# Optimization experiments

Measured on AMD Instinct MI355X. Metric: run time of the kernel, lower is better.

The kernel has to match this reference:

```python
import jax, jax.numpy as jnp
import numpy as np

RADIUS = 1.0
NSAMPLE = 1024  # num_votes
EPS = 1e-5     # BatchNorm eps


def _bn2(x, gamma, beta):
    # BatchNorm over [B, C, NS]: stats per channel across (batch, sample)
    m = jnp.mean(x, axis=(0, 2), keepdims=True)
    v = jnp.var(x, axis=(0, 2), keepdims=True)
    return gamma[None, :, None] * (x - m) * jax.lax.rsqrt(v + EPS) + beta[None, :, None]


def _bn1(x, gamma, beta):
    # BatchNorm over [B, C] (conv1d head with length 1): stats across batch
    m = jnp.mean(x, axis=0, keepdims=True)
    v = jnp.var(x, axis=0, keepdims=True)
    return gamma[None, :] * (x - m) * jax.lax.rsqrt(v + EPS) + beta[None, :]


def setup_inputs() -> dict:
    key = jax.random.key(0)
    ks = jax.random.split(key, 16)
    B, N, C = 8, 65536, 256
    def w(k, o, i):
        return jax.random.normal(k, (o, i), jnp.float32) * (1.0 / np.sqrt(i))
    inp = {
        'xyz': jax.random.normal(ks[0], (B, N, 3), jnp.float32),
        'features': jax.random.normal(ks[1], (B, C, N), jnp.float32),
        # shared MLP (conv2d 1x1 + BN + ReLU) x3, input channels = C+3 (use_xyz)
        'w1': w(ks[2], 128, C + 3), 'b1': jnp.zeros(128), 'g1': jnp.ones(128), 'be1': jnp.zeros(128),
        'w2': w(ks[3], 128, 128),   'b2': jnp.zeros(128), 'g2': jnp.ones(128), 'be2': jnp.zeros(128),
        'w3': w(ks[4], 128, 128),   'b3': jnp.zeros(128), 'g3': jnp.ones(128), 'be3': jnp.zeros(128),
        # conv1d head
        'hw1': w(ks[5], 128, 128), 'hb1': jnp.zeros(128), 'hg1': jnp.ones(128), 'hbe1': jnp.zeros(128),
        'hw2': w(ks[6], 128, 128), 'hb2': jnp.zeros(128), 'hg2': jnp.ones(128), 'hbe2': jnp.zeros(128),
        'hw3': w(ks[7], 12, 128),  'hb3': jnp.zeros(12),
    }
    return inp


def reference(xyz, features, w1, b1, g1, be1, w2, b2, g2, be2, w3, b3, g3, be3,
              hw1, hb1, hg1, hbe1, hw2, hb2, hg2, hbe2, hw3, hb3):
    B, N, _ = xyz.shape
    # FPS with npoint=1 deterministically selects point 0
    center = xyz[:, 0, :]                                   # [B,3]
    d2 = jnp.sum((xyz - center[:, None, :]) ** 2, axis=-1)   # [B,N]
    mask = d2 < RADIUS * RADIUS
    ar = jnp.arange(N)
    # ball query: first NSAMPLE in-radius indices (index order), pad with first hit
    order = jnp.argsort(jnp.where(mask, ar, N + ar), axis=1)[:, :NSAMPLE]  # [B,NS]
    valid = jnp.take_along_axis(mask, order, axis=1)
    inds = jnp.where(valid, order, order[:, :1])              # [B,NS]
    g_xyz = (jnp.take_along_axis(xyz, inds[:, :, None], axis=1) - center[:, None, :]) / RADIUS  # [B,NS,3]
    g_feat = jax.vmap(lambda f, i: f[:, i])(features, inds)    # [B,C,NS]
    g = jnp.concatenate([jnp.swapaxes(g_xyz, 1, 2), g_feat], axis=1)  # [B,C+3,NS]

    def mlp(x, w, b, gm, bt):
        y = jnp.einsum('oc,bcn->bon', w, x) + b[None, :, None]
        return jax.nn.relu(_bn2(y, gm, bt))

    h = mlp(g, w1, b1, g1, be1)
    h = mlp(h, w2, b2, g2, be2)
    h = mlp(h, w3, b3, g3, be3)
    f = jnp.max(h, axis=2)                                    # [B,128] maxpool over nsample

    net = jax.nn.relu(_bn1(f @ hw1.T + hb1, hg1, hbe1))
    net = jax.nn.relu(_bn1(net @ hw2.T + hb2, hg2, hbe2))
    net = net @ hw3.T + hb3                                   # [B,12]

    center_out = center + net[:, 0:3]
    size = net[:, 3:6]
    rot_6d = net[:, 6:12]
    return (center_out, size, rot_6d)
```

## Files before the change

### kernel.cpp

```cpp
#include <hip/hip_runtime.h>
#include <hip/hip_bf16.h>
#include <stdint.h>

#define BATCH 8
#define NPTS  65536
#define CFEAT 256
#define K1    259
#define CH    128
#define NS    1024
#define EPSF  1e-5f

__global__ __launch_bounds__(1024) void k_select(const float* __restrict__ xyz,
                                                 int* __restrict__ inds,
                                                 float* __restrict__ center) {
  int b = blockIdx.x;
  int tid = threadIdx.x;
  int lane = tid & 63, wid = tid >> 6;
  const float* xb = xyz + (size_t)b * NPTS * 3;
  float cx = xb[0], cy = xb[1], cz = xb[2];
  if (tid < 3) center[b * 3 + tid] = xb[tid];

  __shared__ int wcnt[16];
  int total = 0;
  int* ib = inds + b * NS;

  for (int base = 0; base < NPTS; base += 1024) {
    int i = base + tid;
    float dx = xb[(size_t)i * 3 + 0] - cx;
    float dy = xb[(size_t)i * 3 + 1] - cy;
    float dz = xb[(size_t)i * 3 + 2] - cz;
    float d2 = dx * dx + dy * dy + dz * dz;
    bool pred = d2 < 1.0f;
    unsigned long long bal = __ballot(pred);
    if (lane == 0) wcnt[wid] = (int)__popcll(bal);
    __syncthreads();
    int woff = 0, itot = 0;
#pragma unroll
    for (int w = 0; w < 16; ++w) {
      int c = wcnt[w];
      if (w < wid) woff += c;
      itot += c;
    }
    int pos = total + woff + (int)__popcll(bal & ((1ull << lane) - 1ull));
    if (pred && pos < NS) ib[pos] = i;
    total += itot;
    __syncthreads();
    if (total >= NS) break;
  }
  for (int j = total + tid; j < NS; j += 1024) ib[j] = 0;
}

__global__ __launch_bounds__(256) void k_gather(const float* __restrict__ xyz,
                                                const float* __restrict__ feat,
                                                const int* __restrict__ inds,
                                                const float* __restrict__ center,
                                                float* __restrict__ g) {
  int bc = blockIdx.x;
  int b = bc / K1, c = bc % K1;
  const int* ib = inds + b * NS;
  float* gout = g + ((size_t)b * K1 + c) * NS;
  if (c < 3) {
    float cen = center[b * 3 + c];
    for (int n = threadIdx.x; n < NS; n += 256) {
      int id = ib[n];
      gout[n] = xyz[((size_t)b * NPTS + id) * 3 + c] - cen;
    }
  } else {
    const float* fr = feat + ((size_t)b * CFEAT + (c - 3)) * NPTS;
    for (int n = threadIdx.x; n < NS; n += 256) {
      gout[n] = fr[ib[n]];
    }
  }
}

__global__ __launch_bounds__(256) void k_gemm1(const float* __restrict__ g,
                                               const float* __restrict__ W,
                                               const float* __restrict__ bias,
                                               float* __restrict__ y) {
  __shared__ float Ws[128 * 32];
  __shared__ float Xs[32 * 64];
  int b = blockIdx.y;
  int n0 = blockIdx.x * 64;
  int tid = threadIdx.x;
  int tx = tid & 15, ty = tid >> 4;
  float acc[8][4];
#pragma unroll
  for (int r = 0; r < 8; ++r)
#pragma unroll
    for (int j = 0; j < 4; ++j) acc[r][j] = 0.f;

  const float* xb = g + (size_t)b * K1 * NS;
  for (int k0 = 0; k0 < K1; k0 += 32) {
    for (int e = tid; e < 128 * 32; e += 256) {
      int o = e >> 5, kk = e & 31;
      int k = k0 + kk;
      Ws[e] = (k < K1) ? W[o * K1 + k] : 0.f;
    }
    for (int e = tid; e < 32 * 64; e += 256) {
      int kk = e >> 6, j = e & 63;
      int k = k0 + kk;
      Xs[e] = (k < K1) ? xb[(size_t)k * NS + n0 + j] : 0.f;
    }
    __syncthreads();
#pragma unroll
    for (int kk = 0; kk < 32; ++kk) {
      float4 xv = *(const float4*)&Xs[kk * 64 + tx * 4];
#pragma unroll
      for (int r = 0; r < 8; ++r) {
        float a = Ws[(ty * 8 + r) * 32 + kk];
        acc[r][0] += a * xv.x;
        acc[r][1] += a * xv.y;
        acc[r][2] += a * xv.z;
        acc[r][3] += a * xv.w;
      }
    }
    __syncthreads();
  }
#pragma unroll
  for (int r = 0; r < 8; ++r) {
    int o = ty * 8 + r;
    float bs = bias[o];
    float4 v = make_float4(acc[r][0] + bs, acc[r][1] + bs, acc[r][2] + bs, acc[r][3] + bs);
    *(float4*)&y[((size_t)b * CH + o) * NS + n0 + tx * 4] = v;
  }
}

__global__ __launch_bounds__(256) void k_gemm23(const float* __restrict__ x,
                                                const float* __restrict__ scale,
                                                const float* __restrict__ shift,
                                                const float* __restrict__ W,
                                                const float* __restrict__ bias,
                                                float* __restrict__ y) {
  __shared__ float Ws[128 * 32];
  __shared__ float Xs[32 * 64];
  int b = blockIdx.y;
  int n0 = blockIdx.x * 64;
  int tid = threadIdx.x;
  int tx = tid & 15, ty = tid >> 4;
  float acc[8][4];
#pragma unroll
  for (int r = 0; r < 8; ++r)
#pragma unroll
    for (int j = 0; j < 4; ++j) acc[r][j] = 0.f;

  for (int k0 = 0; k0 < 128; k0 += 32) {
    for (int e = tid; e < 128 * 32; e += 256) {
      int o = e >> 5, kk = e & 31;
      Ws[e] = W[o * 128 + k0 + kk];
    }
    for (int e = tid; e < 32 * 64; e += 256) {
      int kk = e >> 6, j = e & 63;
      int k = k0 + kk;
      float v = x[((size_t)b * CH + k) * NS + n0 + j];
      Xs[e] = fmaxf(scale[k] * v + shift[k], 0.f);
    }
    __syncthreads();
#pragma unroll
    for (int kk = 0; kk < 32; ++kk) {
      float4 xv = *(const float4*)&Xs[kk * 64 + tx * 4];
#pragma unroll
      for (int r = 0; r < 8; ++r) {
        float a = Ws[(ty * 8 + r) * 32 + kk];
        acc[r][0] += a * xv.x;
        acc[r][1] += a * xv.y;
        acc[r][2] += a * xv.z;
        acc[r][3] += a * xv.w;
      }
    }
    __syncthreads();
  }
#pragma unroll
  for (int r = 0; r < 8; ++r) {
    int o = ty * 8 + r;
    float bs = bias[o];
    float4 v = make_float4(acc[r][0] + bs, acc[r][1] + bs, acc[r][2] + bs, acc[r][3] + bs);
    *(float4*)&y[((size_t)b * CH + o) * NS + n0 + tx * 4] = v;
  }
}

__global__ __launch_bounds__(256) void k_stats(const float* __restrict__ y,
                                               const float* __restrict__ gamma,
                                               const float* __restrict__ beta,
                                               float* __restrict__ scale,
                                               float* __restrict__ shift) {
  int c = blockIdx.x;
  int tid = threadIdx.x;
  float s = 0.f, sq = 0.f;
  for (int b = 0; b < BATCH; ++b) {
    const float* yr = y + ((size_t)b * CH + c) * NS;
    for (int n = tid; n < NS; n += 256) {
      float v = yr[n];
      s += v;
      sq += v * v;
    }
  }
  __shared__ float rs[256];
  __shared__ float rq[256];
  rs[tid] = s;
  rq[tid] = sq;
  __syncthreads();
  for (int st = 128; st > 0; st >>= 1) {
    if (tid < st) {
      rs[tid] += rs[tid + st];
      rq[tid] += rq[tid + st];
    }
    __syncthreads();
  }
  if (tid == 0) {
    const float inv = 1.f / (BATCH * NS);
    float mean = rs[0] * inv;
    float var = rq[0] * inv - mean * mean;
    if (var < 0.f) var = 0.f;
    float r = rsqrtf(var + EPSF);
    float sc = gamma[c] * r;
    scale[c] = sc;
    shift[c] = beta[c] - mean * sc;
  }
}

__global__ __launch_bounds__(256) void k_max(const float* __restrict__ y,
                                             const float* __restrict__ scale,
                                             const float* __restrict__ shift,
                                             float* __restrict__ f) {
  int idx = blockIdx.x;
  int c = idx & (CH - 1);
  const float* yr = y + (size_t)idx * NS;
  float sc = scale[c], sh = shift[c];
  float m = -1e30f;
  for (int n = threadIdx.x; n < NS; n += 256) m = fmaxf(m, sc * yr[n] + sh);
#pragma unroll
  for (int o = 32; o > 0; o >>= 1) m = fmaxf(m, __shfl_down(m, o, 64));
  __shared__ float wm[4];
  if ((threadIdx.x & 63) == 0) wm[threadIdx.x >> 6] = m;
  __syncthreads();
  if (threadIdx.x == 0) {
    m = fmaxf(fmaxf(wm[0], wm[1]), fmaxf(wm[2], wm[3]));
    f[idx] = fmaxf(m, 0.f);
  }
}

__global__ __launch_bounds__(128) void k_head(const float* __restrict__ f,
                                              const float* __restrict__ hw1, const float* __restrict__ hb1,
                                              const float* __restrict__ hg1, const float* __restrict__ hbe1,
                                              const float* __restrict__ hw2, const float* __restrict__ hb2,
                                              const float* __restrict__ hg2, const float* __restrict__ hbe2,
                                              const float* __restrict__ hw3, const float* __restrict__ hb3,
                                              const float* __restrict__ center,
                                              float* __restrict__ out) {
  __shared__ float A[BATCH * 128];
  __shared__ float Bm[BATCH * 128];
  int c = threadIdx.x;
  for (int b = 0; b < BATCH; ++b) A[b * 128 + c] = f[b * 128 + c];
  __syncthreads();

  {
    float v[BATCH];
    float bs = hb1[c];
#pragma unroll
    for (int b = 0; b < BATCH; ++b) v[b] = bs;
    for (int k = 0; k < 128; ++k) {
      float w = hw1[c * 128 + k];
#pragma unroll
      for (int b = 0; b < BATCH; ++b) v[b] += A[b * 128 + k] * w;
    }
    float m = 0.f;
#pragma unroll
    for (int b = 0; b < BATCH; ++b) m += v[b];
    m *= (1.f / BATCH);
    float var = 0.f;
#pragma unroll
    for (int b = 0; b < BATCH; ++b) { float d = v[b] - m; var += d * d; }
    var *= (1.f / BATCH);
    float r = rsqrtf(var + EPSF);
    float ga = hg1[c], be = hbe1[c];
#pragma unroll
    for (int b = 0; b < BATCH; ++b)
      Bm[b * 128 + c] = fmaxf(ga * (v[b] - m) * r + be, 0.f);
  }
  __syncthreads();

  {
    float v[BATCH];
    float bs = hb2[c];
#pragma unroll
    for (int b = 0; b < BATCH; ++b) v[b] = bs;
    for (int k = 0; k < 128; ++k) {
      float w = hw2[c * 128 + k];
#pragma unroll
      for (int b = 0; b < BATCH; ++b) v[b] += Bm[b * 128 + k] * w;
    }
    float m = 0.f;
#pragma unroll
    for (int b = 0; b < BATCH; ++b) m += v[b];
    m *= (1.f / BATCH);
    float var = 0.f;
#pragma unroll
    for (int b = 0; b < BATCH; ++b) { float d = v[b] - m; var += d * d; }
    var *= (1.f / BATCH);
    float r = rsqrtf(var + EPSF);
    float ga = hg2[c], be = hbe2[c];
#pragma unroll
    for (int b = 0; b < BATCH; ++b)
      A[b * 128 + c] = fmaxf(ga * (v[b] - m) * r + be, 0.f);
  }
  __syncthreads();

  if (c < 96) {
    int b = c / 12, j = c % 12;
    float o = hb3[j];
    for (int k = 0; k < 128; ++k) o += A[b * 128 + k] * hw3[j * 128 + k];
    if (j < 3)      out[b * 3 + j] = center[b * 3 + j] + o;
    else if (j < 6) out[24 + b * 3 + (j - 3)] = o;
    else            out[48 + b * 6 + (j - 6)] = o;
  }
}

extern "C" void kernel_launch(void* const* d_in, const int* in_sizes, int n_in,
                              void* d_out, int out_size, void* d_ws, size_t ws_size,
                              hipStream_t stream) {
  const float* xyz  = (const float*)d_in[0];
  const float* feat = (const float*)d_in[1];
  const float* w1   = (const float*)d_in[2];
  const float* b1   = (const float*)d_in[3];
  const float* ga1  = (const float*)d_in[4];
  const float* be1  = (const float*)d_in[5];
  const float* w2   = (const float*)d_in[6];
  const float* b2   = (const float*)d_in[7];
  const float* ga2  = (const float*)d_in[8];
  const float* be2  = (const float*)d_in[9];
  const float* w3   = (const float*)d_in[10];
  const float* b3   = (const float*)d_in[11];
  const float* ga3  = (const float*)d_in[12];
  const float* be3  = (const float*)d_in[13];
  const float* hw1  = (const float*)d_in[14];
  const float* hb1  = (const float*)d_in[15];
  const float* hg1  = (const float*)d_in[16];
  const float* hbe1 = (const float*)d_in[17];
  const float* hw2  = (const float*)d_in[18];
  const float* hb2  = (const float*)d_in[19];
  const float* hg2  = (const float*)d_in[20];
  const float* hbe2 = (const float*)d_in[21];
  const float* hw3  = (const float*)d_in[22];
  const float* hb3  = (const float*)d_in[23];
  float* out = (float*)d_out;

  char* ws = (char*)d_ws;
  size_t off = 0;
  auto alloc = [&](size_t bytes) -> void* {
    void* p = ws + off;
    off = (off + bytes + 255) & ~(size_t)255;
    return p;
  };
  int*   inds   = (int*)alloc((size_t)BATCH * NS * 4);
  float* center = (float*)alloc(BATCH * 3 * 4);
  float* sc1    = (float*)alloc(CH * 4);
  float* sh1    = (float*)alloc(CH * 4);
  float* sc2    = (float*)alloc(CH * 4);
  float* sh2    = (float*)alloc(CH * 4);
  float* sc3    = (float*)alloc(CH * 4);
  float* sh3    = (float*)alloc(CH * 4);
  float* fmaxb  = (float*)alloc(BATCH * CH * 4);
  float* g      = (float*)alloc((size_t)BATCH * K1 * NS * 4);
  float* y1     = (float*)alloc((size_t)BATCH * CH * NS * 4);
  float* y2     = g;
  float* y3     = y1;

  k_select<<<dim3(BATCH), dim3(1024), 0, stream>>>(xyz, inds, center);
  k_gather<<<dim3(BATCH * K1), dim3(256), 0, stream>>>(xyz, feat, inds, center, g);
  k_gemm1<<<dim3(NS / 64, BATCH), dim3(256), 0, stream>>>(g, w1, b1, y1);
  k_stats<<<dim3(CH), dim3(256), 0, stream>>>(y1, ga1, be1, sc1, sh1);
  k_gemm23<<<dim3(NS / 64, BATCH), dim3(256), 0, stream>>>(y1, sc1, sh1, w2, b2, y2);
  k_stats<<<dim3(CH), dim3(256), 0, stream>>>(y2, ga2, be2, sc2, sh2);
  k_gemm23<<<dim3(NS / 64, BATCH), dim3(256), 0, stream>>>(y2, sc2, sh2, w3, b3, y3);
  k_stats<<<dim3(CH), dim3(256), 0, stream>>>(y3, ga3, be3, sc3, sh3);
  k_max<<<dim3(BATCH * CH), dim3(256), 0, stream>>>(y3, sc3, sh3, fmaxb);
  k_head<<<dim3(1), dim3(128), 0, stream>>>(fmaxb, hw1, hb1, hg1, hbe1,
                                            hw2, hb2, hg2, hbe2, hw3, hb3,
                                            center, out);
}
```

Baseline: 884.4 us.

## Fuse gather into first GEMM and BN statistics into GEMM epilogues

The separate gather kernel is removed: the first GEMM now loads xyz and feature values straight through the selected indices into shared memory. The standalone per-channel stats kernels are also removed; each GEMM epilogue reduces sums and squared sums with wave shuffles and atomically adds them to a zeroed buffer, and the consumers fold these into scale and shift. GEMM tiles shrink to 32 columns with a transposed, padded weight tile that is read as float4, doubling the block count. The head's dot products are vectorised. The cost is scattered gather reads inside the GEMM K-loop and float atomics whose summation order varies between runs.

```diff
diff --git a/kernel.cpp b/kernel.cpp
--- a/kernel.cpp
+++ b/kernel.cpp
@@ -9,6 +9,7 @@
 #define CH    128
 #define NS    1024
 #define EPSF  1e-5f
+#define INVN  (1.0f / (BATCH * NS))
 
 __global__ __launch_bounds__(1024) void k_select(const float* __restrict__ xyz,
                                                  int* __restrict__ inds,
@@ -50,182 +51,169 @@
   for (int j = total + tid; j < NS; j += 1024) ib[j] = 0;
 }
 
-__global__ __launch_bounds__(256) void k_gather(const float* __restrict__ xyz,
-                                                const float* __restrict__ feat,
-                                                const int* __restrict__ inds,
-                                                const float* __restrict__ center,
-                                                float* __restrict__ g) {
-  int bc = blockIdx.x;
-  int b = bc / K1, c = bc % K1;
-  const int* ib = inds + b * NS;
-  float* gout = g + ((size_t)b * K1 + c) * NS;
-  if (c < 3) {
-    float cen = center[b * 3 + c];
-    for (int n = threadIdx.x; n < NS; n += 256) {
-      int id = ib[n];
-      gout[n] = xyz[((size_t)b * NPTS + id) * 3 + c] - cen;
-    }
-  } else {
-    const float* fr = feat + ((size_t)b * CFEAT + (c - 3)) * NPTS;
-    for (int n = threadIdx.x; n < NS; n += 256) {
-      gout[n] = fr[ib[n]];
-    }
-  }
-}
-
-__global__ __launch_bounds__(256) void k_gemm1(const float* __restrict__ g,
+__device__ __forceinline__ void store_and_stats(float* __restrict__ yb,
+                                                float* __restrict__ sums,
+                                                const float* __restrict__ bias,
+                                                float acc[4][4],
+                                                int n0, int tx, int ty) {
+#pragma unroll
+  for (int r = 0; r < 4; ++r) {
+    int o = ty * 4 + r;
+    float bs = bias[o];
+    float4 v = make_float4(acc[r][0] + bs, acc[r][1] + bs,
+                           acc[r][2] + bs, acc[r][3] + bs);
+    *(float4*)&yb[(size_t)o * NS + n0 + tx * 4] = v;
+    float s = v.x + v.y + v.z + v.w;
+    float q = v.x * v.x + v.y * v.y + v.z * v.z + v.w * v.w;
+    s += __shfl_xor(s, 1, 64); q += __shfl_xor(q, 1, 64);
+    s += __shfl_xor(s, 2, 64); q += __shfl_xor(q, 2, 64);
+    s += __shfl_xor(s, 4, 64); q += __shfl_xor(q, 4, 64);
+    if (tx == 0) {
+      atomicAdd(&sums[o], s);
+      atomicAdd(&sums[CH + o], q);
+    }
+  }
+}
+
+__global__ __launch_bounds__(256) void k_gemm1(const float* __restrict__ xyz,
+                                               const float* __restrict__ feat,
+                                               const int* __restrict__ inds,
+                                               const float* __restrict__ center,
                                                const float* __restrict__ W,
                                                const float* __restrict__ bias,
-                                               float* __restrict__ y) {
-  __shared__ float Ws[128 * 32];
-  __shared__ float Xs[32 * 64];
+                                               float* __restrict__ y,
+                                               float* __restrict__ sums) {
+  __shared__ float Ws[32][132];
+  __shared__ float Xs[32][36];
+  __shared__ int   ids[32];
+  __shared__ float cenl[3];
   int b = blockIdx.y;
-  int n0 = blockIdx.x * 64;
+  int n0 = blockIdx.x * 32;
   int tid = threadIdx.x;
-  int tx = tid & 15, ty = tid >> 4;
-  float acc[8][4];
-#pragma unroll
-  for (int r = 0; r < 8; ++r)
+  if (tid < 32) ids[tid] = inds[b * NS + n0 + tid];
+  if (tid < 3)  cenl[tid] = center[b * 3 + tid];
+  __syncthreads();
+
+  int tx = tid & 7, ty = tid >> 3;
+  float acc[4][4];
+#pragma unroll
+  for (int r = 0; r < 4; ++r)
 #pragma unroll
     for (int j = 0; j < 4; ++j) acc[r][j] = 0.f;
 
-  const float* xb = g + (size_t)b * K1 * NS;
+  const float* featb = feat + (size_t)b * CFEAT * NPTS;
+  const float* xyzb  = xyz + (size_t)b * NPTS * 3;
+
   for (int k0 = 0; k0 < K1; k0 += 32) {
-    for (int e = tid; e < 128 * 32; e += 256) {
+#pragma unroll
+    for (int i = 0; i < 16; ++i) {
+      int e = tid + 256 * i;
       int o = e >> 5, kk = e & 31;
       int k = k0 + kk;
-      Ws[e] = (k < K1) ? W[o * K1 + k] : 0.f;
-    }
-    for (int e = tid; e < 32 * 64; e += 256) {
-      int kk = e >> 6, j = e & 63;
+      Ws[kk][o] = (k < K1) ? W[o * K1 + k] : 0.f;
+    }
+#pragma unroll
+    for (int i = 0; i < 4; ++i) {
+      int e = tid + 256 * i;
+      int kk = e >> 5, j = e & 31;
       int k = k0 + kk;
-      Xs[e] = (k < K1) ? xb[(size_t)k * NS + n0 + j] : 0.f;
+      float v = 0.f;
+      int id = ids[j];
+      if (k < 3)        v = xyzb[(size_t)id * 3 + k] - cenl[k];
+      else if (k < K1)  v = featb[(size_t)(k - 3) * NPTS + id];
+      Xs[kk][j] = v;
     }
     __syncthreads();
 #pragma unroll
     for (int kk = 0; kk < 32; ++kk) {
-      float4 xv = *(const float4*)&Xs[kk * 64 + tx * 4];
-#pragma unroll
-      for (int r = 0; r < 8; ++r) {
-        float a = Ws[(ty * 8 + r) * 32 + kk];
-        acc[r][0] += a * xv.x;
-        acc[r][1] += a * xv.y;
-        acc[r][2] += a * xv.z;
-        acc[r][3] += a * xv.w;
-      }
-    }
-    __syncthreads();
-  }
-#pragma unroll
-  for (int r = 0; r < 8; ++r) {
-    int o = ty * 8 + r;
-    float bs = bias[o];
-    float4 v = make_float4(acc[r][0] + bs, acc[r][1] + bs, acc[r][2] + bs, acc[r][3] + bs);
-    *(float4*)&y[((size_t)b * CH + o) * NS + n0 + tx * 4] = v;
-  }
+      float4 xv = *(const float4*)&Xs[kk][tx * 4];
+      float4 wv = *(const float4*)&Ws[kk][ty * 4];
+      acc[0][0] += wv.x * xv.x; acc[0][1] += wv.x * xv.y; acc[0][2] += wv.x * xv.z; acc[0][3] += wv.x * xv.w;
+      acc[1][0] += wv.y * xv.x; acc[1][1] += wv.y * xv.y; acc[1][2] += wv.y * xv.z; acc[1][3] += wv.y * xv.w;
+      acc[2][0] += wv.z * xv.x; acc[2][1] += wv.z * xv.y; acc[2][2] += wv.z * xv.z; acc[2][3] += wv.z * xv.w;
+      acc[3][0] += wv.w * xv.x; acc[3][1] += wv.w * xv.y; acc[3][2] += wv.w * xv.z; acc[3][3] += wv.w * xv.w;
+    }
+    __syncthreads();
+  }
+  store_and_stats(y + (size_t)b * CH * NS, sums, bias, acc, n0, tx, ty);
 }
 
 __global__ __launch_bounds__(256) void k_gemm23(const float* __restrict__ x,
-                                                const float* __restrict__ scale,
-                                                const float* __restrict__ shift,
+                                                const float* __restrict__ sums_prev,
+                                                const float* __restrict__ gamma,
+                                                const float* __restrict__ beta,
                                                 const float* __restrict__ W,
                                                 const float* __restrict__ bias,
-                                                float* __restrict__ y) {
-  __shared__ float Ws[128 * 32];
-  __shared__ float Xs[32 * 64];
+                                                float* __restrict__ y,
+                                                float* __restrict__ sums_out) {
+  __shared__ float Ws[32][132];
+  __shared__ float Xs[32][36];
+  __shared__ float scl[CH], shf[CH];
   int b = blockIdx.y;
-  int n0 = blockIdx.x * 64;
+  int n0 = blockIdx.x * 32;
   int tid = threadIdx.x;
-  int tx = tid & 15, ty = tid >> 4;
-  float acc[8][4];
-#pragma unroll
-  for (int r = 0; r < 8; ++r)
+  if (tid < CH) {
+    float s = sums_prev[tid], q = sums_prev[CH + tid];
+    float mean = s * INVN;
+    float var = fmaxf(q * INVN - mean * mean, 0.f);
+    float sc = gamma[tid] * rsqrtf(var + EPSF);
+    scl[tid] = sc;
+    shf[tid] = beta[tid] - mean * sc;
+  }
+  __syncthreads();
+
+  int tx = tid & 7, ty = tid >> 3;
+  float acc[4][4];
+#pragma unroll
+  for (int r = 0; r < 4; ++r)
 #pragma unroll
     for (int j = 0; j < 4; ++j) acc[r][j] = 0.f;
 
-  for (int k0 = 0; k0 < 128; k0 += 32) {
-    for (int e = tid; e < 128 * 32; e += 256) {
+  const float* xb = x + (size_t)b * CH * NS;
+
+  for (int k0 = 0; k0 < CH; k0 += 32) {
+#pragma unroll
+    for (int i = 0; i < 16; ++i) {
+      int e = tid + 256 * i;
       int o = e >> 5, kk = e & 31;
-      Ws[e] = W[o * 128 + k0 + kk];
-    }
-    for (int e = tid; e < 32 * 64; e += 256) {
-      int kk = e >> 6, j = e & 63;
+      Ws[kk][o] = W[o * CH + k0 + kk];
+    }
+#pragma unroll
+    for (int i = 0; i < 4; ++i) {
+      int e = tid + 256 * i;
+      int kk = e >> 5, j = e & 31;
       int k = k0 + kk;
-      float v = x[((size_t)b * CH + k) * NS + n0 + j];
-      Xs[e] = fmaxf(scale[k] * v + shift[k], 0.f);
+      float v = xb[(size_t)k * NS + n0 + j];
+      Xs[kk][j] = fmaxf(scl[k] * v + shf[k], 0.f);
     }
     __syncthreads();
 #pragma unroll
     for (int kk = 0; kk < 32; ++kk) {
-      float4 xv = *(const float4*)&Xs[kk * 64 + tx * 4];
-#pragma unroll
-      for (int r = 0; r < 8; ++r) {
-        float a = Ws[(ty * 8 + r) * 32 + kk];
-        acc[r][0] += a * xv.x;
-        acc[r][1] += a * xv.y;
-        acc[r][2] += a * xv.z;
-        acc[r][3] += a * xv.w;
-      }
-    }
-    __syncthreads();
-  }
-#pragma unroll
-  for (int r = 0; r < 8; ++r) {
-    int o = ty * 8 + r;
-    float bs = bias[o];
-    float4 v = make_float4(acc[r][0] + bs, acc[r][1] + bs, acc[r][2] + bs, acc[r][3] + bs);
-    *(float4*)&y[((size_t)b * CH + o) * NS + n0 + tx * 4] = v;
-  }
-}
-
-__global__ __launch_bounds__(256) void k_stats(const float* __restrict__ y,
-                                               const float* __restrict__ gamma,
-                                               const float* __restrict__ beta,
-                                               float* __restrict__ scale,
-                                               float* __restrict__ shift) {
-  int c = blockIdx.x;
-  int tid = threadIdx.x;
-  float s = 0.f, sq = 0.f;
-  for (int b = 0; b < BATCH; ++b) {
-    const float* yr = y + ((size_t)b * CH + c) * NS;
-    for (int n = tid; n < NS; n += 256) {
-      float v = yr[n];
-      s += v;
-      sq += v * v;
-    }
-  }
-  __shared__ float rs[256];
-  __shared__ float rq[256];
-  rs[tid] = s;
-  rq[tid] = sq;
-  __syncthreads();
-  for (int st = 128; st > 0; st >>= 1) {
-    if (tid < st) {
-      rs[tid] += rs[tid + st];
-      rq[tid] += rq[tid + st];
-    }
-    __syncthreads();
-  }
-  if (tid == 0) {
-    const float inv = 1.f / (BATCH * NS);
-    float mean = rs[0] * inv;
-    float var = rq[0] * inv - mean * mean;
-    if (var < 0.f) var = 0.f;
-    float r = rsqrtf(var + EPSF);
-    float sc = gamma[c] * r;
-    scale[c] = sc;
-    shift[c] = beta[c] - mean * sc;
-  }
+      float4 xv = *(const float4*)&Xs[kk][tx * 4];
+      float4 wv = *(const float4*)&Ws[kk][ty * 4];
+      acc[0][0] += wv.x * xv.x; acc[0][1] += wv.x * xv.y; acc[0][2] += wv.x * xv.z; acc[0][3] += wv.x * xv.w;
+      acc[1][0] += wv.y * xv.x; acc[1][1] += wv.y * xv.y; acc[1][2] += wv.y * xv.z; acc[1][3] += wv.y * xv.w;
+      acc[2][0] += wv.z * xv.x; acc[2][1] += wv.z * xv.y; acc[2][2] += wv.z * xv.z; acc[2][3] += wv.z * xv.w;
+      acc[3][0] += wv.w * xv.x; acc[3][1] += wv.w * xv.y; acc[3][2] += wv.w * xv.z; acc[3][3] += wv.w * xv.w;
+    }
+    __syncthreads();
+  }
+  store_and_stats(y + (size_t)b * CH * NS, sums_out, bias, acc, n0, tx, ty);
 }
 
 __global__ __launch_bounds__(256) void k_max(const float* __restrict__ y,
-                                             const float* __restrict__ scale,
-                                             const float* __restrict__ shift,
+                                             const float* __restrict__ sums,
+                                             const float* __restrict__ gamma,
+                                             const float* __restrict__ beta,
                                              float* __restrict__ f) {
   int idx = blockIdx.x;
   int c = idx & (CH - 1);
+  float s = sums[c], q = sums[CH + c];
+  float mean = s * INVN;
+  float var = fmaxf(q * INVN - mean * mean, 0.f);
+  float sc = gamma[c] * rsqrtf(var + EPSF);
+  float sh = beta[c] - mean * sc;
   const float* yr = y + (size_t)idx * NS;
-  float sc = scale[c], sh = shift[c];
   float m = -1e30f;
   for (int n = threadIdx.x; n < NS; n += 256) m = fmaxf(m, sc * yr[n] + sh);
 #pragma unroll
@@ -258,10 +246,14 @@
     float bs = hb1[c];
 #pragma unroll
     for (int b = 0; b < BATCH; ++b) v[b] = bs;
-    for (int k = 0; k < 128; ++k) {
-      float w = hw1[c * 128 + k];
-#pragma unroll
-      for (int b = 0; b < BATCH; ++b) v[b] += A[b * 128 + k] * w;
+    const float4* w4 = (const float4*)hw1 + c * 32;
+    for (int k4 = 0; k4 < 32; ++k4) {
+      float4 w = w4[k4];
+#pragma unroll
+      for (int b = 0; b < BATCH; ++b) {
+        const float* Ar = &A[b * 128 + k4 * 4];
+        v[b] += Ar[0] * w.x + Ar[1] * w.y + Ar[2] * w.z + Ar[3] * w.w;
+      }
     }
     float m = 0.f;
 #pragma unroll
@@ -284,10 +276,14 @@
     float bs = hb2[c];
 #pragma unroll
     for (int b = 0; b < BATCH; ++b) v[b] = bs;
-    for (int k = 0; k < 128; ++k) {
-      float w = hw2[c * 128 + k];
-#pragma unroll
-      for (int b = 0; b < BATCH; ++b) v[b] += Bm[b * 128 + k] * w;
+    const float4* w4 = (const float4*)hw2 + c * 32;
+    for (int k4 = 0; k4 < 32; ++k4) {
+      float4 w = w4[k4];
+#pragma unroll
+      for (int b = 0; b < BATCH; ++b) {
+        const float* Br = &Bm[b * 128 + k4 * 4];
+        v[b] += Br[0] * w.x + Br[1] * w.y + Br[2] * w.z + Br[3] * w.w;
+      }
     }
     float m = 0.f;
 #pragma unroll
@@ -308,7 +304,12 @@
   if (c < 96) {
     int b = c / 12, j = c % 12;
     float o = hb3[j];
-    for (int k = 0; k < 128; ++k) o += A[b * 128 + k] * hw3[j * 128 + k];
+    const float4* w4 = (const float4*)hw3 + j * 32;
+    for (int k4 = 0; k4 < 32; ++k4) {
+      float4 w = w4[k4];
+      const float* Ar = &A[b * 128 + k4 * 4];
+      o += Ar[0] * w.x + Ar[1] * w.y + Ar[2] * w.z + Ar[3] * w.w;
+    }
     if (j < 3)      out[b * 3 + j] = center[b * 3 + j] + o;
     else if (j < 6) out[24 + b * 3 + (j - 3)] = o;
     else            out[48 + b * 6 + (j - 6)] = o;
@@ -351,29 +352,26 @@
     off = (off + bytes + 255) & ~(size_t)255;
     return p;
   };
+  float* sums1  = (float*)alloc(2 * CH * 4);
+  float* sums2  = (float*)alloc(2 * CH * 4);
+  float* sums3  = (float*)alloc(2 * CH * 4);
   int*   inds   = (int*)alloc((size_t)BATCH * NS * 4);
   float* center = (float*)alloc(BATCH * 3 * 4);
-  float* sc1    = (float*)alloc(CH * 4);
-  float* sh1    = (float*)alloc(CH * 4);
-  float* sc2    = (float*)alloc(CH * 4);
-  float* sh2    = (float*)alloc(CH * 4);
-  float* sc3    = (float*)alloc(CH * 4);
-  float* sh3    = (float*)alloc(CH * 4);
   float* fmaxb  = (float*)alloc(BATCH * CH * 4);
-  float* g      = (float*)alloc((size_t)BATCH * K1 * NS * 4);
   float* y1     = (float*)alloc((size_t)BATCH * CH * NS * 4);
-  float* y2     = g;
+  float* y2     = (float*)alloc((size_t)BATCH * CH * NS * 4);
   float* y3     = y1;
 
+  hipMemsetAsync(sums1, 0, ((char*)center - (char*)sums1), stream);
+
   k_select<<<dim3(BATCH), dim3(1024), 0, stream>>>(xyz, inds, center);
-  k_gather<<<dim3(BATCH * K1), dim3(256), 0, stream>>>(xyz, feat, inds, center, g);
-  k_gemm1<<<dim3(NS / 64, BATCH), dim3(256), 0, stream>>>(g, w1, b1, y1);
-  k_stats<<<dim3(CH), dim3(256), 0, stream>>>(y1, ga1, be1, sc1, sh1);
-  k_gemm23<<<dim3(NS / 64, BATCH), dim3(256), 0, stream>>>(y1, sc1, sh1, w2, b2, y2);
-  k_stats<<<dim3(CH), dim3(256), 0, stream>>>(y2, ga2, be2, sc2, sh2);
-  k_gemm23<<<dim3(NS / 64, BATCH), dim3(256), 0, stream>>>(y2, sc2, sh2, w3, b3, y3);
-  k_stats<<<dim3(CH), dim3(256), 0, stream>>>(y3, ga3, be3, sc3, sh3);
-  k_max<<<dim3(BATCH * CH), dim3(256), 0, stream>>>(y3, sc3, sh3, fmaxb);
+  k_gemm1<<<dim3(NS / 32, BATCH), dim3(256), 0, stream>>>(xyz, feat, inds, center,
+                                                          w1, b1, y1, sums1);
+  k_gemm23<<<dim3(NS / 32, BATCH), dim3(256), 0, stream>>>(y1, sums1, ga1, be1,
+                                                           w2, b2, y2, sums2);
+  k_gemm23<<<dim3(NS / 32, BATCH), dim3(256), 0, stream>>>(y2, sums2, ga2, be2,
+                                                           w3, b3, y3, sums3);
+  k_max<<<dim3(BATCH * CH), dim3(256), 0, stream>>>(y3, sums3, ga3, be3, fmaxb);
   k_head<<<dim3(1), dim3(128), 0, stream>>>(fmaxb, hw1, hb1, hg1, hbe1,
                                             hw2, hb2, hg2, hbe2, hw3, hb3,
                                             center, out);
```

Measured after the change: 849.0 us. 4.0% less time.
